# Kernel optimization log

Measured on AMD Instinct MI355X. Metric: run time of the kernel, lower is better.

## Reference

```python
import jax, jax.numpy as jnp
import numpy as np

V, E, H, DV = 32000, 512, 1024, 512
B, K = 64, 49


def setup_inputs():
    key = jax.random.key(0)
    ks = jax.random.split(key, 16)
    p = lambda i, shape: jax.random.normal(ks[i], shape, dtype=jnp.float32) * 0.02
    return {
        "thought": jax.random.normal(ks[0], (B, H), dtype=jnp.float32),
        "visual_features": jax.random.normal(ks[1], (B, K, DV), dtype=jnp.float32),
        "max_len": 64,
        "embedding": p(2, (V, E)),
        "Wih1": p(3, (4 * H, E)), "Whh1": p(4, (4 * H, H)),
        "bih1": jnp.zeros((4 * H,), jnp.float32), "bhh1": jnp.zeros((4 * H,), jnp.float32),
        "Wih2": p(5, (4 * H, H)), "Whh2": p(6, (4 * H, H)),
        "bih2": jnp.zeros((4 * H,), jnp.float32), "bhh2": jnp.zeros((4 * H,), jnp.float32),
        "Wg1": p(7, (H, H)), "bg1": jnp.zeros((H,), jnp.float32),
        "Wg2": p(8, (1, H)), "bg2": jnp.zeros((1,), jnp.float32),
        "Wo": p(9, (V, H)), "bo": jnp.zeros((V,), jnp.float32),
        "Wv": p(10, (H, DV)), "bv": jnp.zeros((H,), jnp.float32),
        "ln_g": jnp.ones((H,), jnp.float32), "ln_b": jnp.zeros((H,), jnp.float32),
    }


def _lstm_cell(x, h, c, Wih, Whh, bih, bhh):
    # PyTorch LSTM gate order: i, f, g, o
    z = x @ Wih.T + h @ Whh.T + bih + bhh
    i, f, g, o = jnp.split(z, 4, axis=-1)
    c_new = jax.nn.sigmoid(f) * c + jax.nn.sigmoid(i) * jnp.tanh(g)
    h_new = jax.nn.sigmoid(o) * jnp.tanh(c_new)
    return h_new, c_new


def reference(thought, visual_features, max_len, embedding, Wih1, Whh1, bih1, bhh1,
              Wih2, Whh2, bih2, bbh2=None, bih2_dummy=None, **_unused):
    raise RuntimeError('placeholder')


def reference(thought, visual_features, max_len, embedding, Wih1, Whh1, bih1, bhh1,
              Wih2, Whh2, bih2, bhh2, Wg1, bg1, Wg2, bg2, Wo, bo, Wv, bv, ln_g, ln_b):
    Bsz, Hd = thought.shape
    temperature = 0.4  # epoch = 0 -> 0.4 + 0.4*0
    top_p = 0.7        # epoch = 0 -> 0.7 + 0.2*0
    scale = 1.0 / jnp.sqrt(jnp.asarray(Hd, jnp.float32))
    # visual_proj: Linear + LayerNorm (Dropout is identity in eval mode)
    vp = visual_features @ Wv.T + bv
    mu = vp.mean(-1, keepdims=True)
    var = vp.var(-1, keepdims=True)
    vp = (vp - mu) / jnp.sqrt(var + 1e-5) * ln_g + ln_b  # [B,K,H]
    b_idx = jnp.arange(Bsz)
    # carry: (h1,c1,h2,c2, input token, last-3 token history, history validity)
    init = (thought, jnp.zeros_like(thought), thought, jnp.zeros_like(thought),
            jnp.full((Bsz,), 1, jnp.int32),
            jnp.zeros((Bsz, 3), jnp.int32), jnp.zeros((Bsz, 3), jnp.bool_))
    keys = jax.random.split(jax.random.key(42), max_len)

    def step(carry, key):
        h1, c1, h2, c2, inp, hist, histv = carry
        emb = embedding[inp]  # [B,E]
        h1, c1 = _lstm_cell(emb, h1, c1, Wih1, Whh1, bih1, bhh1)
        h2, c2 = _lstm_cell(h1, h2, c2, Wih2, Whh2, bih2, bhh2)
        gate = jax.nn.sigmoid(jnp.tanh(h2 @ Wg1.T + bg1) @ Wg2.T + bg2)  # [B,1]
        out = h2 * gate
        attn = jax.nn.softmax(jnp.einsum('bh,bkh->bk', out, vp) * scale, axis=-1)
        out = out + jnp.einsum('bk,bkh->bh', attn, vp)
        logits = out @ Wo.T + bo  # [B,V]
        # repetition penalty: -2.0 once per UNIQUE token in last-3 history (set semantics via .max)
        pen = jnp.zeros_like(logits).at[b_idx[:, None], hist].max(histv.astype(logits.dtype))
        logits = (logits - 2.0 * pen) / temperature
        # nucleus (top-p) filtering, matching top_k_top_p_filtering with top_k=0
        order = jnp.argsort(-logits, axis=-1)
        sl = jnp.take_along_axis(logits, order, axis=-1)
        cum = jnp.cumsum(jax.nn.softmax(sl, axis=-1), axis=-1)
        rem = cum > top_p
        rem = jnp.concatenate([jnp.zeros_like(rem[:, :1]), rem[:, :-1]], axis=-1)
        mask = jnp.zeros_like(rem).at[b_idx[:, None], order].set(rem)
        logits = jnp.where(mask, -jnp.inf, logits)
        nxt = jax.random.categorical(key, logits).astype(jnp.int32)  # multinomial sample
        hist = jnp.concatenate([hist[:, 1:], nxt[:, None]], axis=1)
        histv = jnp.concatenate([histv[:, 1:], jnp.ones((Bsz, 1), jnp.bool_)], axis=1)
        return (h1, c1, h2, c2, nxt, hist, histv), nxt

    _, toks = jax.lax.scan(step, init, keys)
    return toks.T  # [B, max_len]
```

## Files before the change

kernel.cpp:

```cpp
#include <hip/hip_runtime.h>
#include <hip/hip_bf16.h>
#include <stdint.h>


#define B_   64
#define H_   1024
#define E_   512
#define DV_  512
#define KV_  49
#define V_   32000
#define T_   64

__device__ __forceinline__ uint32_t rotl32(uint32_t x, int r) {
  return (x << r) | (x >> (32 - r));
}
__device__ __forceinline__ void tf2x32(uint32_t k0, uint32_t k1,
                                       uint32_t x0, uint32_t x1,
                                       uint32_t& o0, uint32_t& o1) {
  uint32_t ks0 = k0, ks1 = k1, ks2 = k0 ^ k1 ^ 0x1BD11BDAu;
  x0 += ks0; x1 += ks1;
#define RND_(r) { x0 += x1; x1 = rotl32(x1, r) ^ x0; }
  RND_(13) RND_(15) RND_(26) RND_(6)  x0 += ks1; x1 += ks2 + 1u;
  RND_(17) RND_(29) RND_(16) RND_(24) x0 += ks2; x1 += ks0 + 2u;
  RND_(13) RND_(15) RND_(26) RND_(6)  x0 += ks0; x1 += ks1 + 3u;
  RND_(17) RND_(29) RND_(16) RND_(24) x0 += ks1; x1 += ks2 + 4u;
  RND_(13) RND_(15) RND_(26) RND_(6)  x0 += ks2; x1 += ks0 + 5u;
#undef RND_
  o0 = x0; o1 = x1;
}

__device__ __forceinline__ unsigned key_of(float f) {
  unsigned u = __float_as_uint(f);
  return (u & 0x80000000u) ? ~u : (u | 0x80000000u);
}
__device__ __forceinline__ float sigf(float x) { return 1.0f / (1.0f + expf(-x)); }

template <int BN, int TM, int TN, int NTHR>
__global__ __launch_bounds__(NTHR)
void gemm_dq(const float* __restrict__ A0, int lda0, const float* __restrict__ W0,
             int ldw0, int K0, float* __restrict__ out0, int ldo0, int nt0,
             const float* __restrict__ A1, int lda1, const float* __restrict__ W1,
             int ldw1, int K1, float* __restrict__ out1, int ldo1) {
  constexpr int LD = 36;
  constexpr int ROWS = 64 + BN;
  constexpr int NF4 = ROWS * 8 / NTHR;
  constexpr int BUFST = ROWS * LD;
  constexpr int CG = BN / TN;
  static_assert(ROWS * 8 % NTHR == 0, "staging divisibility");
  static_assert((64 / TM) * CG == NTHR, "thread grid");
  static_assert(TN == 4, "float4 epilogue");
  __shared__ __align__(16) float S[2][ROWS][LD];

  const int tid = threadIdx.x;
  const int bx = blockIdx.x;
  const float* A; const float* W; float* out;
  int lda, ldw, K, ldo, n0;
  if (bx < nt0) { A = A0; W = W0; out = out0; lda = lda0; ldw = ldw0; K = K0; ldo = ldo0; n0 = bx * BN; }
  else          { A = A1; W = W1; out = out1; lda = lda1; ldw = ldw1; K = K1; ldo = ldo1; n0 = (bx - nt0) * BN; }
  const int m0 = blockIdx.y * 64;
  const int tc = tid % CG, tr = tid / CG;

  const float* gp[NF4];
  float* lp[NF4];
#pragma unroll
  for (int q = 0; q < NF4; ++q) {
    int l = tid + q * NTHR;
    int r = l >> 3, c4 = l & 7;
    gp[q] = (l < 512) ? (A + (m0 + r) * lda + c4 * 4)
                      : (W + (n0 + (r - 64)) * ldw + c4 * 4);
    lp[q] = &S[0][r][(c4 ^ ((r >> 2) & 7)) << 2];
  }

  float4 pre[NF4];
#pragma unroll
  for (int q = 0; q < NF4; ++q) pre[q] = *(const float4*)gp[q];
#pragma unroll
  for (int q = 0; q < NF4; ++q) *(float4*)lp[q] = pre[q];
  __syncthreads();

  float acc[TM][TN] = {};
  const int nch = K >> 5;
  for (int c = 0; c < nch; ++c) {
    const bool more = (c + 1 < nch);
    if (more) {
      const int kc = (c + 1) << 5;
#pragma unroll
      for (int q = 0; q < NF4; ++q) pre[q] = *(const float4*)(gp[q] + kc);
    }
    const float* Sb = &S[c & 1][0][0];
#pragma unroll
    for (int kk = 0; kk < 8; ++kk) {
      float4 a4[TM], w4[TN];
#pragma unroll
      for (int i = 0; i < TM; ++i) {
        int m = tr * TM + i;
        a4[i] = *(const float4*)(Sb + m * LD + ((kk ^ ((m >> 2) & 7)) << 2));
      }
#pragma unroll
      for (int j = 0; j < TN; ++j) {
        int rw = 64 + tc * TN + j;
        w4[j] = *(const float4*)(Sb + rw * LD + ((kk ^ ((rw >> 2) & 7)) << 2));
      }
#pragma unroll
      for (int i = 0; i < TM; ++i)
#pragma unroll
        for (int j = 0; j < TN; ++j) {
          acc[i][j] = fmaf(a4[i].x, w4[j].x, acc[i][j]);
          acc[i][j] = fmaf(a4[i].y, w4[j].y, acc[i][j]);
          acc[i][j] = fmaf(a4[i].z, w4[j].z, acc[i][j]);
          acc[i][j] = fmaf(a4[i].w, w4[j].w, acc[i][j]);
        }
    }
    if (more) {
      const int bo = ((c + 1) & 1) * BUFST;
#pragma unroll
      for (int q = 0; q < NF4; ++q) *(float4*)(lp[q] + bo) = pre[q];
    }
    __syncthreads();
  }

#pragma unroll
  for (int i = 0; i < TM; ++i) {
    float4 o;
    o.x = acc[i][0]; o.y = acc[i][1]; o.z = acc[i][2]; o.w = acc[i][3];
    *(float4*)&out[(m0 + tr * TM + i) * ldo + n0 + tc * TN] = o;
  }
}

__global__ __launch_bounds__(256)
void ln_vp(float* __restrict__ vp, const float* __restrict__ bv,
           const float* __restrict__ g, const float* __restrict__ bt) {
  int row = blockIdx.x, tid = threadIdx.x;
  __shared__ float buf[H_];
  __shared__ float red[256];
  float* p = vp + (long long)row * H_;
  for (int h = tid; h < H_; h += 256) buf[h] = __fadd_rn(p[h], bv[h]);
  __syncthreads();
  float s = 0;
  for (int h = tid; h < H_; h += 256) s += buf[h];
  red[tid] = s; __syncthreads();
  for (int off = 128; off > 0; off >>= 1) { if (tid < off) red[tid] += red[tid + off]; __syncthreads(); }
  float mu = red[0] / (float)H_;
  __syncthreads();
  float vs = 0;
  for (int h = tid; h < H_; h += 256) { float d = buf[h] - mu; vs += d * d; }
  red[tid] = vs; __syncthreads();
  for (int off = 128; off > 0; off >>= 1) { if (tid < off) red[tid] += red[tid + off]; __syncthreads(); }
  float var = red[0] / (float)H_;
  float sq = sqrtf(var + 1e-5f);
  for (int h = tid; h < H_; h += 256) {
    float nrm = __fdiv_rn(__fsub_rn(buf[h], mu), sq);
    p[h] = __fadd_rn(__fmul_rn(nrm, g[h]), bt[h]);
  }
}

__global__ __launch_bounds__(256)
void lstm_cell2(const float* __restrict__ dx, const float* __restrict__ dh,
                const float* __restrict__ bih, const float* __restrict__ bhh,
                float* __restrict__ c,
                float* __restrict__ hA, int ldA, float* __restrict__ hB, int ldB) {
  int idx = blockIdx.x * 256 + threadIdx.x;
  int b = idx >> 10, h = idx & 1023;
  float z[4];
#pragma unroll
  for (int g = 0; g < 4; g++) {
    int j = g * 1024 + h;
    float s = __fadd_rn(dx[b * 4096 + j], dh[b * 4096 + j]);
    s = __fadd_rn(s, bih[j]);
    s = __fadd_rn(s, bhh[j]);
    z[g] = s;
  }
  float fc = __fmul_rn(sigf(z[1]), c[idx]);
  float ig = __fmul_rn(sigf(z[0]), tanhf(z[2]));
  float cn = __fadd_rn(fc, ig);
  float hn = __fmul_rn(sigf(z[3]), tanhf(cn));
  c[idx] = cn;
  hA[(long long)b * ldA + h] = hn;
  hB[(long long)b * ldB + h] = hn;
}

__global__ __launch_bounds__(256)
void gate_attn(const float* __restrict__ dg, const float* __restrict__ bg1,
               const float* __restrict__ Wg2, const float* __restrict__ bg2,
               const float* __restrict__ h2buf, const float* __restrict__ vp,
               float* __restrict__ ctx) {
  int b = blockIdx.x, tid = threadIdx.x;
  __shared__ float t1[H_], outv[H_], attn[64];
  __shared__ float gate_s;
  for (int h = tid; h < H_; h += 256)
    t1[h] = tanhf(__fadd_rn(dg[b * H_ + h], bg1[h]));
  __syncthreads();
  if (tid == 0) {
    float s = 0;
    for (int h = 0; h < H_; h++) s = fmaf(t1[h], Wg2[h], s);
    gate_s = sigf(__fadd_rn(s, bg2[0]));
  }
  __syncthreads();
  float gate = gate_s;
  for (int h = tid; h < H_; h += 256) outv[h] = __fmul_rn(h2buf[b * H_ + h], gate);
  __syncthreads();
  if (tid < KV_) {
    const float* vrow = vp + ((long long)b * KV_ + tid) * H_;
    float a = 0;
    for (int h = 0; h < H_; h++) a = fmaf(outv[h], vrow[h], a);
    attn[tid] = __fmul_rn(a, 0.03125f);
  }
  __syncthreads();
  if (tid == 0) {
    float m = -INFINITY;
    for (int k = 0; k < KV_; k++) m = fmaxf(m, attn[k]);
    float ss = 0;
    for (int k = 0; k < KV_; k++) { attn[k] = expf(attn[k] - m); ss += attn[k]; }
    for (int k = 0; k < KV_; k++) attn[k] = __fdiv_rn(attn[k], ss);
  }
  __syncthreads();
  for (int h = tid; h < H_; h += 256) {
    float acc = 0;
    for (int k = 0; k < KV_; k++) acc = fmaf(attn[k], vp[((long long)b * KV_ + k) * H_ + h], acc);
    ctx[b * H_ + h] = __fadd_rn(outv[h], acc);
  }
}

__global__ __launch_bounds__(256)
void init_state(const float* __restrict__ thought, const float* __restrict__ embedding,
                float* c1, float* c2, float* xcat1, float* xcat2,
                int* hist, int* histv) {
  int i = blockIdx.x * 256 + threadIdx.x;
  if (i < B_ * H_) {
    int b = i >> 10, h = i & 1023;
    c1[i] = 0.f; c2[i] = 0.f;
    float th = thought[i];
    xcat1[b * (E_ + H_) + E_ + h] = th;
    xcat2[b * (2 * H_) + H_ + h] = th;
    if (h < E_) xcat1[b * (E_ + H_) + h] = embedding[E_ + h];
  }
  if (i < B_ * 3) { hist[i] = 0; histv[i] = 0; }
}

__global__ __launch_bounds__(1024)
void sample_kernel(const float* __restrict__ dlog, const float* __restrict__ bo,
                   float* __restrict__ Lbuf, float* __restrict__ Ebuf,
                   int* __restrict__ hist, int* __restrict__ histv,
                   const float* __restrict__ embedding, float* __restrict__ xcat1,
                   int* __restrict__ outTok, int t) {
  int b = blockIdx.x, tid = threadIdx.x;
  __shared__ float redf[1024];
  __shared__ int   redi[1024];
  __shared__ unsigned long long binS[256], suf[256];
  __shared__ unsigned binC[256];
  __shared__ int jstar_s;
  __shared__ unsigned long long carry_s;
  __shared__ unsigned prefix_s;

  int hh0 = hist[b * 3 + 0], hh1 = hist[b * 3 + 1], hh2 = hist[b * 3 + 2];
  int p0 = histv[b * 3 + 0] ? hh0 : -1;
  int p1 = histv[b * 3 + 1] ? hh1 : -1;
  int p2 = histv[b * 3 + 2] ? hh2 : -1;
  const float* pa = dlog + (long long)b * V_;
  float* L = Lbuf + (long long)b * V_;
  float* E = Ebuf + (long long)b * V_;

  float lm = -INFINITY;
  for (int v = tid; v < V_; v += 1024) {
    float raw = __fadd_rn(pa[v], bo[v]);
    if (v == p0 || v == p1 || v == p2) raw = __fsub_rn(raw, 2.0f);
    float l = __fdiv_rn(raw, 0.4f);
    L[v] = l;
    lm = fmaxf(lm, l);
  }
  redf[tid] = lm; __syncthreads();
  for (int off = 512; off > 0; off >>= 1) { if (tid < off) redf[tid] = fmaxf(redf[tid], redf[tid + off]); __syncthreads(); }
  float m = redf[0];
  __syncthreads();

  float ls = 0;
  for (int v = tid; v < V_; v += 1024) { float e = expf(L[v] - m); E[v] = e; ls += e; }
  redf[tid] = ls; __syncthreads();
  for (int off = 512; off > 0; off >>= 1) { if (tid < off) redf[tid] += redf[tid + off]; __syncthreads(); }
  float Z = redf[0];
  __syncthreads();

  const double SC = 17592186044416.0;
  const unsigned long long B0 =
      (unsigned long long)(0.699999988079071044921875 * 17592186044416.0);
  if (tid == 0) { carry_s = 0ull; prefix_s = 0u; }
  __syncthreads();
  for (int pass = 0; pass < 4; pass++) {
    int shift = 24 - 8 * pass;
    unsigned maskk = (pass == 0) ? 0u : (0xFFFFFFFFu << (shift + 8));
    if (tid < 256) { binS[tid] = 0ull; binC[tid] = 0u; }
    __syncthreads();
    unsigned pref = prefix_s;
    unsigned long long carry = carry_s;
    for (int v = tid; v < V_; v += 1024) {
      unsigned key = key_of(L[v]);
      if ((key & maskk) == pref) {
        unsigned bin = (key >> shift) & 255u;
        unsigned long long S = (unsigned long long)((double)(E[v] / Z) * SC);
        atomicAdd(&binS[bin], S);
        atomicAdd(&binC[bin], 1u);
      }
    }
    __syncthreads();
    if (tid < 256) suf[tid] = binS[tid];
    __syncthreads();
    for (int off = 1; off < 256; off <<= 1) {
      unsigned long long add = 0ull;
      if (tid < 256 && tid + off < 256) add = suf[tid + off];
      __syncthreads();
      if (tid < 256) suf[tid] += add;
      __syncthreads();
    }
    if (tid == 0) jstar_s = 256;
    __syncthreads();
    if (tid < 256 && binC[tid] > 0u) {
      unsigned long long A = carry + ((tid < 255) ? suf[tid + 1] : 0ull);
      if (A <= B0) atomicMin(&jstar_s, tid);
    }
    __syncthreads();
    if (tid == 0) {
      int j = jstar_s;
      carry_s = carry + ((j < 255) ? suf[j + 1] : 0ull);
      prefix_s = pref | (((unsigned)j) << shift);
    }
    __syncthreads();
  }
  unsigned Kstar = prefix_s;

  unsigned kt0, kt1;
  tf2x32(0u, 42u, 0u, (unsigned)t, kt0, kt1);

  float bestv = -INFINITY; int besti = 0x7fffffff;
  for (int v = tid; v < V_; v += 1024) {
    float l = L[v];
    if (key_of(l) >= Kstar) {
      unsigned r0, r1;
      tf2x32(kt0, kt1, 0u, (unsigned)(b * V_ + v), r0, r1);
      unsigned bits = r0 ^ r1;
      float u = __uint_as_float((bits >> 9) | 0x3f800000u) - 1.0f;
      u = fmaxf(u, 1.17549435e-38f);
      float gum = -logf(-logf(u));
      float val = __fadd_rn(l, gum);
      if (val > bestv) { bestv = val; besti = v; }
    }
  }
  redf[tid] = bestv; redi[tid] = besti; __syncthreads();
  for (int off = 512; off > 0; off >>= 1) {
    if (tid < off) {
      float ov = redf[tid + off]; int oi = redi[tid + off];
      if (ov > redf[tid] || (ov == redf[tid] && oi < redi[tid])) { redf[tid] = ov; redi[tid] = oi; }
    }
    __syncthreads();
  }
  int tok = redi[0];
  if (tid == 0) {
    outTok[b * T_ + t] = tok;
    hist[b * 3 + 0] = hh1; hist[b * 3 + 1] = hh2; hist[b * 3 + 2] = tok;
    int v1 = histv[b * 3 + 1], v2 = histv[b * 3 + 2];
    histv[b * 3 + 0] = v1; histv[b * 3 + 1] = v2; histv[b * 3 + 2] = 1;
  }
  for (int k = tid; k < E_; k += 1024)
    xcat1[b * (E_ + H_) + k] = embedding[(long long)tok * E_ + k];
}

extern "C" void kernel_launch(void* const* d_in, const int* in_sizes, int n_in,
                              void* d_out, int out_size, void* d_ws, size_t ws_size,
                              hipStream_t stream) {
  const float* thought   = (const float*)d_in[0];
  const float* visf      = (const float*)d_in[1];
  const float* embedding = (const float*)d_in[3];
  const float* Wih1 = (const float*)d_in[4];
  const float* Whh1 = (const float*)d_in[5];
  const float* bih1 = (const float*)d_in[6];
  const float* bhh1 = (const float*)d_in[7];
  const float* Wih2 = (const float*)d_in[8];
  const float* Whh2 = (const float*)d_in[9];
  const float* bih2 = (const float*)d_in[10];
  const float* bhh2 = (const float*)d_in[11];
  const float* Wg1  = (const float*)d_in[12];
  const float* bg1  = (const float*)d_in[13];
  const float* Wg2  = (const float*)d_in[14];
  const float* bg2  = (const float*)d_in[15];
  const float* Wo   = (const float*)d_in[16];
  const float* bo   = (const float*)d_in[17];
  const float* Wv   = (const float*)d_in[18];
  const float* bv   = (const float*)d_in[19];
  const float* ln_g = (const float*)d_in[20];
  const float* ln_b = (const float*)d_in[21];
  int* outTok = (int*)d_out;

  float* ws = (float*)d_ws;
  long long off = 0;
  float* vp    = ws + off; off += (long long)B_ * KV_ * H_;
  float* xcat1 = ws + off; off += B_ * (E_ + H_);
  float* xcat2 = ws + off; off += B_ * (2 * H_);
  float* c1    = ws + off; off += B_ * H_;
  float* c2    = ws + off; off += B_ * H_;
  float* h2buf = ws + off; off += B_ * H_;
  float* ctx   = ws + off; off += B_ * H_;
  float* dx    = ws + off; off += (long long)B_ * 4096;
  float* dh    = ws + off; off += (long long)B_ * 4096;
  float* dg    = ws + off; off += (long long)B_ * H_;
  float* dlog  = ws + off; off += (long long)B_ * V_;
  float* Lbuf  = ws + off; off += (long long)B_ * V_;
  float* Ebuf  = ws + off; off += (long long)B_ * V_;
  int* hist  = (int*)(ws + off); off += 256;
  int* histv = (int*)(ws + off); off += 256;

  init_state<<<256, 256, 0, stream>>>(thought, embedding, c1, c2, xcat1, xcat2, hist, histv);

  gemm_dq<128, 8, 4, 256><<<dim3(8, KV_), 256, 0, stream>>>(
      visf, DV_, Wv, DV_, DV_, vp, H_, 8,
      visf, DV_, Wv, DV_, DV_, vp, H_);
  ln_vp<<<B_ * KV_, 256, 0, stream>>>(vp, bv, ln_g, ln_b);

  for (int t = 0; t < T_; t++) {
    gemm_dq<32, 4, 4, 128><<<dim3(256, 1), 128, 0, stream>>>(
        xcat1, E_ + H_, Wih1, E_, E_, dx, 4096, 128,
        xcat1 + E_, E_ + H_, Whh1, H_, H_, dh, 4096);
    lstm_cell2<<<256, 256, 0, stream>>>(dx, dh, bih1, bhh1, c1,
                                        xcat1 + E_, E_ + H_, xcat2, 2 * H_);
    gemm_dq<32, 4, 4, 128><<<dim3(256, 1), 128, 0, stream>>>(
        xcat2, 2 * H_, Wih2, H_, H_, dx, 4096, 128,
        xcat2 + H_, 2 * H_, Whh2, H_, H_, dh, 4096);
    lstm_cell2<<<256, 256, 0, stream>>>(dx, dh, bih2, bhh2, c2,
                                        h2buf, H_, xcat2 + H_, 2 * H_);
    gemm_dq<32, 4, 4, 128><<<dim3(32, 1), 128, 0, stream>>>(
        h2buf, H_, Wg1, H_, H_, dg, H_, 32,
        h2buf, H_, Wg1, H_, H_, dg, H_);
    gate_attn<<<B_, 256, 0, stream>>>(dg, bg1, Wg2, bg2, h2buf, vp, ctx);
    gemm_dq<128, 8, 4, 256><<<dim3(250, 1), 256, 0, stream>>>(
        ctx, H_, Wo, H_, H_, dlog, V_, 250,
        ctx, H_, Wo, H_, H_, dlog, V_);
    sample_kernel<<<B_, 1024, 0, stream>>>(dlog, bo, Lbuf, Ebuf, hist, histv,
                                           embedding, xcat1, outTok, t);
  }
}
```

Measured before the change: 31.30 ms.

## Fuse all decode steps into one persistent megakernel with grid barriers

Replaces the per-timestep sequence of separate kernel launches (GEMMs, LSTM cells, gate/attention, sampling) with a single persistent kernel of 256 blocks that synchronises phases through a software global barrier. Sampling is split across four blocks per batch row, with partial histograms and argmax results exchanged through workspace buffers. The aim is to remove hundreds of launch overheads and tail gaps across the 64-step recurrence. In exchange, each block is limited to 256 threads and one block per CU, and the kernel depends on all 256 blocks being co-resident for the spin barrier to avoid deadlock.

```diff
diff --git a/kernel.cpp b/kernel.cpp
--- a/kernel.cpp
+++ b/kernel.cpp
@@ -1,5 +1,4 @@
 #include <hip/hip_runtime.h>
-#include <hip/hip_bf16.h>
 #include <stdint.h>
 
 
@@ -10,6 +9,7 @@
 #define KV_  49
 #define V_   32000
 #define T_   64
+#define NBLK 256
 
 __device__ __forceinline__ uint32_t rotl32(uint32_t x, int r) {
   return (x << r) | (x >> (32 - r));
@@ -35,12 +35,32 @@
 }
 __device__ __forceinline__ float sigf(float x) { return 1.0f / (1.0f + expf(-x)); }
 
+__device__ __forceinline__ void gsync(unsigned* bar) {
+  __syncthreads();
+  if (threadIdx.x == 0) {
+    __threadfence();
+    unsigned g = __hip_atomic_load(&bar[1], __ATOMIC_RELAXED, __HIP_MEMORY_SCOPE_AGENT);
+    unsigned a = __hip_atomic_fetch_add(&bar[0], 1u, __ATOMIC_ACQ_REL, __HIP_MEMORY_SCOPE_AGENT);
+    if (a + 1u == (unsigned)NBLK) {
+      __hip_atomic_store(&bar[0], 0u, __ATOMIC_RELAXED, __HIP_MEMORY_SCOPE_AGENT);
+      __hip_atomic_store(&bar[1], g + 1u, __ATOMIC_RELEASE, __HIP_MEMORY_SCOPE_AGENT);
+    } else {
+      while (__hip_atomic_load(&bar[1], __ATOMIC_ACQUIRE, __HIP_MEMORY_SCOPE_AGENT) == g)
+        __builtin_amdgcn_s_sleep(2);
+    }
+  }
+  __syncthreads();
+}
+
+__global__ void bar_init(unsigned* bar) {
+  if (threadIdx.x < 2) bar[threadIdx.x] = 0u;
+}
+
 template <int BN, int TM, int TN, int NTHR>
-__global__ __launch_bounds__(NTHR)
-void gemm_dq(const float* __restrict__ A0, int lda0, const float* __restrict__ W0,
-             int ldw0, int K0, float* __restrict__ out0, int ldo0, int nt0,
-             const float* __restrict__ A1, int lda1, const float* __restrict__ W1,
-             int ldw1, int K1, float* __restrict__ out1, int ldo1) {
+__device__ void gemm_tile(int tid, float* Sb0, int n0, int m0,
+                          const float* __restrict__ A, int lda,
+                          const float* __restrict__ W, int ldw, int K,
+                          float* __restrict__ out, int ldo) {
   constexpr int LD = 36;
   constexpr int ROWS = 64 + BN;
   constexpr int NF4 = ROWS * 8 / NTHR;
@@ -49,390 +69,480 @@
   static_assert(ROWS * 8 % NTHR == 0, "staging divisibility");
   static_assert((64 / TM) * CG == NTHR, "thread grid");
   static_assert(TN == 4, "float4 epilogue");
-  __shared__ __align__(16) float S[2][ROWS][LD];
-
-  const int tid = threadIdx.x;
-  const int bx = blockIdx.x;
-  const float* A; const float* W; float* out;
-  int lda, ldw, K, ldo, n0;
-  if (bx < nt0) { A = A0; W = W0; out = out0; lda = lda0; ldw = ldw0; K = K0; ldo = ldo0; n0 = bx * BN; }
-  else          { A = A1; W = W1; out = out1; lda = lda1; ldw = ldw1; K = K1; ldo = ldo1; n0 = (bx - nt0) * BN; }
-  const int m0 = blockIdx.y * 64;
+  const bool act = tid < NTHR;
   const int tc = tid % CG, tr = tid / CG;
-
   const float* gp[NF4];
   float* lp[NF4];
-#pragma unroll
-  for (int q = 0; q < NF4; ++q) {
-    int l = tid + q * NTHR;
-    int r = l >> 3, c4 = l & 7;
-    gp[q] = (l < 512) ? (A + (m0 + r) * lda + c4 * 4)
-                      : (W + (n0 + (r - 64)) * ldw + c4 * 4);
-    lp[q] = &S[0][r][(c4 ^ ((r >> 2) & 7)) << 2];
-  }
-
   float4 pre[NF4];
-#pragma unroll
-  for (int q = 0; q < NF4; ++q) pre[q] = *(const float4*)gp[q];
-#pragma unroll
-  for (int q = 0; q < NF4; ++q) *(float4*)lp[q] = pre[q];
+  if (act) {
+#pragma unroll
+    for (int q = 0; q < NF4; ++q) {
+      int l = tid + q * NTHR;
+      int r = l >> 3, c4 = l & 7;
+      gp[q] = (l < 512) ? (A + (m0 + r) * lda + c4 * 4)
+                        : (W + (n0 + (r - 64)) * ldw + c4 * 4);
+      lp[q] = Sb0 + r * LD + ((c4 ^ ((r >> 2) & 7)) << 2);
+    }
+#pragma unroll
+    for (int q = 0; q < NF4; ++q) pre[q] = *(const float4*)gp[q];
+#pragma unroll
+    for (int q = 0; q < NF4; ++q) *(float4*)lp[q] = pre[q];
+  }
   __syncthreads();
-
   float acc[TM][TN] = {};
   const int nch = K >> 5;
   for (int c = 0; c < nch; ++c) {
     const bool more = (c + 1 < nch);
-    if (more) {
+    if (act && more) {
       const int kc = (c + 1) << 5;
 #pragma unroll
       for (int q = 0; q < NF4; ++q) pre[q] = *(const float4*)(gp[q] + kc);
     }
-    const float* Sb = &S[c & 1][0][0];
-#pragma unroll
-    for (int kk = 0; kk < 8; ++kk) {
-      float4 a4[TM], w4[TN];
-#pragma unroll
-      for (int i = 0; i < TM; ++i) {
-        int m = tr * TM + i;
-        a4[i] = *(const float4*)(Sb + m * LD + ((kk ^ ((m >> 2) & 7)) << 2));
-      }
-#pragma unroll
-      for (int j = 0; j < TN; ++j) {
-        int rw = 64 + tc * TN + j;
-        w4[j] = *(const float4*)(Sb + rw * LD + ((kk ^ ((rw >> 2) & 7)) << 2));
-      }
-#pragma unroll
-      for (int i = 0; i < TM; ++i)
+    if (act) {
+      const float* Sb = Sb0 + (c & 1) * BUFST;
+#pragma unroll
+      for (int kk = 0; kk < 8; ++kk) {
+        float4 a4[TM], w4[TN];
+#pragma unroll
+        for (int i = 0; i < TM; ++i) {
+          int m = tr * TM + i;
+          a4[i] = *(const float4*)(Sb + m * LD + ((kk ^ ((m >> 2) & 7)) << 2));
+        }
 #pragma unroll
         for (int j = 0; j < TN; ++j) {
-          acc[i][j] = fmaf(a4[i].x, w4[j].x, acc[i][j]);
-          acc[i][j] = fmaf(a4[i].y, w4[j].y, acc[i][j]);
-          acc[i][j] = fmaf(a4[i].z, w4[j].z, acc[i][j]);
-          acc[i][j] = fmaf(a4[i].w, w4[j].w, acc[i][j]);
-        }
-    }
-    if (more) {
-      const int bo = ((c + 1) & 1) * BUFST;
-#pragma unroll
-      for (int q = 0; q < NF4; ++q) *(float4*)(lp[q] + bo) = pre[q];
+          int rw = 64 + tc * TN + j;
+          w4[j] = *(const float4*)(Sb + rw * LD + ((kk ^ ((rw >> 2) & 7)) << 2));
+        }
+#pragma unroll
+        for (int i = 0; i < TM; ++i)
+#pragma unroll
+          for (int j = 0; j < TN; ++j) {
+            acc[i][j] = fmaf(a4[i].x, w4[j].x, acc[i][j]);
+            acc[i][j] = fmaf(a4[i].y, w4[j].y, acc[i][j]);
+            acc[i][j] = fmaf(a4[i].z, w4[j].z, acc[i][j]);
+            acc[i][j] = fmaf(a4[i].w, w4[j].w, acc[i][j]);
+          }
+      }
+    }
+    if (act && more) {
+      const int bo2 = ((c + 1) & 1) * BUFST;
+#pragma unroll
+      for (int q = 0; q < NF4; ++q) *(float4*)(lp[q] + bo2) = pre[q];
     }
     __syncthreads();
   }
-
-#pragma unroll
-  for (int i = 0; i < TM; ++i) {
-    float4 o;
-    o.x = acc[i][0]; o.y = acc[i][1]; o.z = acc[i][2]; o.w = acc[i][3];
-    *(float4*)&out[(m0 + tr * TM + i) * ldo + n0 + tc * TN] = o;
-  }
-}
-
-__global__ __launch_bounds__(256)
-void ln_vp(float* __restrict__ vp, const float* __restrict__ bv,
-           const float* __restrict__ g, const float* __restrict__ bt) {
-  int row = blockIdx.x, tid = threadIdx.x;
-  __shared__ float buf[H_];
-  __shared__ float red[256];
-  float* p = vp + (long long)row * H_;
-  for (int h = tid; h < H_; h += 256) buf[h] = __fadd_rn(p[h], bv[h]);
-  __syncthreads();
-  float s = 0;
-  for (int h = tid; h < H_; h += 256) s += buf[h];
-  red[tid] = s; __syncthreads();
-  for (int off = 128; off > 0; off >>= 1) { if (tid < off) red[tid] += red[tid + off]; __syncthreads(); }
-  float mu = red[0] / (float)H_;
-  __syncthreads();
-  float vs = 0;
-  for (int h = tid; h < H_; h += 256) { float d = buf[h] - mu; vs += d * d; }
-  red[tid] = vs; __syncthreads();
-  for (int off = 128; off > 0; off >>= 1) { if (tid < off) red[tid] += red[tid + off]; __syncthreads(); }
-  float var = red[0] / (float)H_;
-  float sq = sqrtf(var + 1e-5f);
-  for (int h = tid; h < H_; h += 256) {
-    float nrm = __fdiv_rn(__fsub_rn(buf[h], mu), sq);
-    p[h] = __fadd_rn(__fmul_rn(nrm, g[h]), bt[h]);
-  }
-}
-
-__global__ __launch_bounds__(256)
-void lstm_cell2(const float* __restrict__ dx, const float* __restrict__ dh,
-                const float* __restrict__ bih, const float* __restrict__ bhh,
-                float* __restrict__ c,
-                float* __restrict__ hA, int ldA, float* __restrict__ hB, int ldB) {
-  int idx = blockIdx.x * 256 + threadIdx.x;
-  int b = idx >> 10, h = idx & 1023;
-  float z[4];
-#pragma unroll
-  for (int g = 0; g < 4; g++) {
-    int j = g * 1024 + h;
-    float s = __fadd_rn(dx[b * 4096 + j], dh[b * 4096 + j]);
-    s = __fadd_rn(s, bih[j]);
-    s = __fadd_rn(s, bhh[j]);
-    z[g] = s;
-  }
-  float fc = __fmul_rn(sigf(z[1]), c[idx]);
-  float ig = __fmul_rn(sigf(z[0]), tanhf(z[2]));
-  float cn = __fadd_rn(fc, ig);
-  float hn = __fmul_rn(sigf(z[3]), tanhf(cn));
-  c[idx] = cn;
-  hA[(long long)b * ldA + h] = hn;
-  hB[(long long)b * ldB + h] = hn;
-}
-
-__global__ __launch_bounds__(256)
-void gate_attn(const float* __restrict__ dg, const float* __restrict__ bg1,
-               const float* __restrict__ Wg2, const float* __restrict__ bg2,
-               const float* __restrict__ h2buf, const float* __restrict__ vp,
-               float* __restrict__ ctx) {
-  int b = blockIdx.x, tid = threadIdx.x;
-  __shared__ float t1[H_], outv[H_], attn[64];
-  __shared__ float gate_s;
-  for (int h = tid; h < H_; h += 256)
-    t1[h] = tanhf(__fadd_rn(dg[b * H_ + h], bg1[h]));
-  __syncthreads();
-  if (tid == 0) {
+  if (act) {
+#pragma unroll
+    for (int i = 0; i < TM; ++i) {
+      float4 o;
+      o.x = acc[i][0]; o.y = acc[i][1]; o.z = acc[i][2]; o.w = acc[i][3];
+      *(float4*)&out[(m0 + tr * TM + i) * ldo + n0 + tc * TN] = o;
+    }
+  }
+}
+
+struct LnLds   { float buf[H_]; float red[256]; };
+struct AttnLds { float t1[H_]; float outv[H_]; float attn[64]; float gate; };
+struct SamLds  {
+  float redf[256]; int redi[256];
+  unsigned long long whist[4][257];
+  unsigned long long suf[256];
+  unsigned long long wq[4];
+  unsigned long long carry;
+  unsigned prefix;
+  int jstar;
+};
+
+struct MegaP {
+  const float *thought, *visf, *embedding;
+  const float *Wih1, *Whh1, *bih1, *bhh1;
+  const float *Wih2, *Whh2, *bih2, *bhh2;
+  const float *Wg1, *bg1, *Wg2, *bg2;
+  const float *Wo, *bo, *Wv, *bv, *ln_g, *ln_b;
+  float *vp, *xcat1, *xcat2, *c1, *c2, *h2buf, *ctx, *dx, *dh, *dg, *dlog, *Lb, *Eb;
+  int *hist, *histv, *outTok;
+  float *pM, *pS, *pGv;
+  int *pGi;
+  unsigned long long *pH;
+  unsigned *bar;
+};
+
+__global__ __launch_bounds__(256, 1)
+void mega(MegaP p) {
+  __shared__ __align__(16) unsigned char LDSU_[55296];
+  float* GS = (float*)LDSU_;
+  const int bx = blockIdx.x;
+  const int tid = threadIdx.x;
+
+  {
+    int i = bx * 256 + tid;
+    if (i < B_ * H_) {
+      int b = i >> 10, h = i & 1023;
+      p.c1[i] = 0.f; p.c2[i] = 0.f;
+      float th = p.thought[i];
+      p.xcat1[b * (E_ + H_) + E_ + h] = th;
+      p.xcat2[b * (2 * H_) + H_ + h] = th;
+      if (h < E_) p.xcat1[b * (E_ + H_) + h] = p.embedding[E_ + h];
+    }
+    if (i < B_ * 3) { p.hist[i] = 0; p.histv[i] = 0; }
+  }
+  for (int s = bx; s < 8 * KV_; s += NBLK)
+    gemm_tile<128, 8, 4, 256>(tid, GS, (s & 7) * 128, (s >> 3) * 64,
+                              p.visf, DV_, p.Wv, DV_, DV_, p.vp, H_);
+  gsync(p.bar);
+
+  for (int row = bx; row < B_ * KV_; row += NBLK) {
+    LnLds& LL = *(LnLds*)LDSU_;
+    float* pp = p.vp + (long long)row * H_;
+    for (int h = tid; h < H_; h += 256) LL.buf[h] = __fadd_rn(pp[h], p.bv[h]);
+    __syncthreads();
     float s = 0;
-    for (int h = 0; h < H_; h++) s = fmaf(t1[h], Wg2[h], s);
-    gate_s = sigf(__fadd_rn(s, bg2[0]));
-  }
-  __syncthreads();
-  float gate = gate_s;
-  for (int h = tid; h < H_; h += 256) outv[h] = __fmul_rn(h2buf[b * H_ + h], gate);
-  __syncthreads();
-  if (tid < KV_) {
-    const float* vrow = vp + ((long long)b * KV_ + tid) * H_;
-    float a = 0;
-    for (int h = 0; h < H_; h++) a = fmaf(outv[h], vrow[h], a);
-    attn[tid] = __fmul_rn(a, 0.03125f);
-  }
-  __syncthreads();
-  if (tid == 0) {
-    float m = -INFINITY;
-    for (int k = 0; k < KV_; k++) m = fmaxf(m, attn[k]);
-    float ss = 0;
-    for (int k = 0; k < KV_; k++) { attn[k] = expf(attn[k] - m); ss += attn[k]; }
-    for (int k = 0; k < KV_; k++) attn[k] = __fdiv_rn(attn[k], ss);
-  }
-  __syncthreads();
-  for (int h = tid; h < H_; h += 256) {
-    float acc = 0;
-    for (int k = 0; k < KV_; k++) acc = fmaf(attn[k], vp[((long long)b * KV_ + k) * H_ + h], acc);
-    ctx[b * H_ + h] = __fadd_rn(outv[h], acc);
-  }
-}
-
-__global__ __launch_bounds__(256)
-void init_state(const float* __restrict__ thought, const float* __restrict__ embedding,
-                float* c1, float* c2, float* xcat1, float* xcat2,
-                int* hist, int* histv) {
-  int i = blockIdx.x * 256 + threadIdx.x;
-  if (i < B_ * H_) {
-    int b = i >> 10, h = i & 1023;
-    c1[i] = 0.f; c2[i] = 0.f;
-    float th = thought[i];
-    xcat1[b * (E_ + H_) + E_ + h] = th;
-    xcat2[b * (2 * H_) + H_ + h] = th;
-    if (h < E_) xcat1[b * (E_ + H_) + h] = embedding[E_ + h];
-  }
-  if (i < B_ * 3) { hist[i] = 0; histv[i] = 0; }
-}
-
-__global__ __launch_bounds__(1024)
-void sample_kernel(const float* __restrict__ dlog, const float* __restrict__ bo,
-                   float* __restrict__ Lbuf, float* __restrict__ Ebuf,
-                   int* __restrict__ hist, int* __restrict__ histv,
-                   const float* __restrict__ embedding, float* __restrict__ xcat1,
-                   int* __restrict__ outTok, int t) {
-  int b = blockIdx.x, tid = threadIdx.x;
-  __shared__ float redf[1024];
-  __shared__ int   redi[1024];
-  __shared__ unsigned long long binS[256], suf[256];
-  __shared__ unsigned binC[256];
-  __shared__ int jstar_s;
-  __shared__ unsigned long long carry_s;
-  __shared__ unsigned prefix_s;
-
-  int hh0 = hist[b * 3 + 0], hh1 = hist[b * 3 + 1], hh2 = hist[b * 3 + 2];
-  int p0 = histv[b * 3 + 0] ? hh0 : -1;
-  int p1 = histv[b * 3 + 1] ? hh1 : -1;
-  int p2 = histv[b * 3 + 2] ? hh2 : -1;
-  const float* pa = dlog + (long long)b * V_;
-  float* L = Lbuf + (long long)b * V_;
-  float* E = Ebuf + (long long)b * V_;
-
-  float lm = -INFINITY;
-  for (int v = tid; v < V_; v += 1024) {
-    float raw = __fadd_rn(pa[v], bo[v]);
-    if (v == p0 || v == p1 || v == p2) raw = __fsub_rn(raw, 2.0f);
-    float l = __fdiv_rn(raw, 0.4f);
-    L[v] = l;
-    lm = fmaxf(lm, l);
-  }
-  redf[tid] = lm; __syncthreads();
-  for (int off = 512; off > 0; off >>= 1) { if (tid < off) redf[tid] = fmaxf(redf[tid], redf[tid + off]); __syncthreads(); }
-  float m = redf[0];
-  __syncthreads();
-
-  float ls = 0;
-  for (int v = tid; v < V_; v += 1024) { float e = expf(L[v] - m); E[v] = e; ls += e; }
-  redf[tid] = ls; __syncthreads();
-  for (int off = 512; off > 0; off >>= 1) { if (tid < off) redf[tid] += redf[tid + off]; __syncthreads(); }
-  float Z = redf[0];
-  __syncthreads();
-
-  const double SC = 17592186044416.0;
-  const unsigned long long B0 =
-      (unsigned long long)(0.699999988079071044921875 * 17592186044416.0);
-  if (tid == 0) { carry_s = 0ull; prefix_s = 0u; }
-  __syncthreads();
-  for (int pass = 0; pass < 4; pass++) {
-    int shift = 24 - 8 * pass;
-    unsigned maskk = (pass == 0) ? 0u : (0xFFFFFFFFu << (shift + 8));
-    if (tid < 256) { binS[tid] = 0ull; binC[tid] = 0u; }
+    for (int h = tid; h < H_; h += 256) s += LL.buf[h];
+    LL.red[tid] = s; __syncthreads();
+    for (int off = 128; off > 0; off >>= 1) { if (tid < off) LL.red[tid] += LL.red[tid + off]; __syncthreads(); }
+    float mu = LL.red[0] / (float)H_;
     __syncthreads();
-    unsigned pref = prefix_s;
-    unsigned long long carry = carry_s;
-    for (int v = tid; v < V_; v += 1024) {
-      unsigned key = key_of(L[v]);
-      if ((key & maskk) == pref) {
-        unsigned bin = (key >> shift) & 255u;
-        unsigned long long S = (unsigned long long)((double)(E[v] / Z) * SC);
-        atomicAdd(&binS[bin], S);
-        atomicAdd(&binC[bin], 1u);
-      }
+    float vs = 0;
+    for (int h = tid; h < H_; h += 256) { float d = LL.buf[h] - mu; vs += d * d; }
+    LL.red[tid] = vs; __syncthreads();
+    for (int off = 128; off > 0; off >>= 1) { if (tid < off) LL.red[tid] += LL.red[tid + off]; __syncthreads(); }
+    float var = LL.red[0] / (float)H_;
+    float sq = sqrtf(var + 1e-5f);
+    for (int h = tid; h < H_; h += 256) {
+      float nrm = __fdiv_rn(__fsub_rn(LL.buf[h], mu), sq);
+      pp[h] = __fadd_rn(__fmul_rn(nrm, p.ln_g[h]), p.ln_b[h]);
     }
     __syncthreads();
-    if (tid < 256) suf[tid] = binS[tid];
-    __syncthreads();
-    for (int off = 1; off < 256; off <<= 1) {
-      unsigned long long add = 0ull;
-      if (tid < 256 && tid + off < 256) add = suf[tid + off];
-      __syncthreads();
-      if (tid < 256) suf[tid] += add;
-      __syncthreads();
-    }
-    if (tid == 0) jstar_s = 256;
-    __syncthreads();
-    if (tid < 256 && binC[tid] > 0u) {
-      unsigned long long A = carry + ((tid < 255) ? suf[tid + 1] : 0ull);
-      if (A <= B0) atomicMin(&jstar_s, tid);
-    }
-    __syncthreads();
-    if (tid == 0) {
-      int j = jstar_s;
-      carry_s = carry + ((j < 255) ? suf[j + 1] : 0ull);
-      prefix_s = pref | (((unsigned)j) << shift);
-    }
-    __syncthreads();
-  }
-  unsigned Kstar = prefix_s;
-
-  unsigned kt0, kt1;
-  tf2x32(0u, 42u, 0u, (unsigned)t, kt0, kt1);
-
-  float bestv = -INFINITY; int besti = 0x7fffffff;
-  for (int v = tid; v < V_; v += 1024) {
-    float l = L[v];
-    if (key_of(l) >= Kstar) {
-      unsigned r0, r1;
-      tf2x32(kt0, kt1, 0u, (unsigned)(b * V_ + v), r0, r1);
-      unsigned bits = r0 ^ r1;
-      float u = __uint_as_float((bits >> 9) | 0x3f800000u) - 1.0f;
-      u = fmaxf(u, 1.17549435e-38f);
-      float gum = -logf(-logf(u));
-      float val = __fadd_rn(l, gum);
-      if (val > bestv) { bestv = val; besti = v; }
-    }
-  }
-  redf[tid] = bestv; redi[tid] = besti; __syncthreads();
-  for (int off = 512; off > 0; off >>= 1) {
-    if (tid < off) {
-      float ov = redf[tid + off]; int oi = redi[tid + off];
-      if (ov > redf[tid] || (ov == redf[tid] && oi < redi[tid])) { redf[tid] = ov; redi[tid] = oi; }
-    }
-    __syncthreads();
-  }
-  int tok = redi[0];
-  if (tid == 0) {
-    outTok[b * T_ + t] = tok;
-    hist[b * 3 + 0] = hh1; hist[b * 3 + 1] = hh2; hist[b * 3 + 2] = tok;
-    int v1 = histv[b * 3 + 1], v2 = histv[b * 3 + 2];
-    histv[b * 3 + 0] = v1; histv[b * 3 + 1] = v2; histv[b * 3 + 2] = 1;
-  }
-  for (int k = tid; k < E_; k += 1024)
-    xcat1[b * (E_ + H_) + k] = embedding[(long long)tok * E_ + k];
+  }
+  gsync(p.bar);
+
+  for (int t = 0; t < T_; ++t) {
+    if (bx < 128)
+      gemm_tile<32, 4, 4, 128>(tid, GS, bx * 32, 0,
+                               p.xcat1, E_ + H_, p.Wih1, E_, E_, p.dx, 4096);
+    else
+      gemm_tile<32, 4, 4, 128>(tid, GS, (bx - 128) * 32, 0,
+                               p.xcat1 + E_, E_ + H_, p.Whh1, H_, H_, p.dh, 4096);
+    gsync(p.bar);
+    {
+      int idx = bx * 256 + tid;
+      int b = idx >> 10, h = idx & 1023;
+      float z[4];
+#pragma unroll
+      for (int g = 0; g < 4; g++) {
+        int j = g * 1024 + h;
+        float s = __fadd_rn(p.dx[b * 4096 + j], p.dh[b * 4096 + j]);
+        s = __fadd_rn(s, p.bih1[j]);
+        s = __fadd_rn(s, p.bhh1[j]);
+        z[g] = s;
+      }
+      float fc = __fmul_rn(sigf(z[1]), p.c1[idx]);
+      float ig = __fmul_rn(sigf(z[0]), tanhf(z[2]));
+      float cn = __fadd_rn(fc, ig);
+      float hn = __fmul_rn(sigf(z[3]), tanhf(cn));
+      p.c1[idx] = cn;
+      p.xcat1[(long long)b * (E_ + H_) + E_ + h] = hn;
+      p.xcat2[(long long)b * (2 * H_) + h] = hn;
+    }
+    gsync(p.bar);
+    if (bx < 128)
+      gemm_tile<32, 4, 4, 128>(tid, GS, bx * 32, 0,
+                               p.xcat2, 2 * H_, p.Wih2, H_, H_, p.dx, 4096);
+    else
+      gemm_tile<32, 4, 4, 128>(tid, GS, (bx - 128) * 32, 0,
+                               p.xcat2 + H_, 2 * H_, p.Whh2, H_, H_, p.dh, 4096);
+    gsync(p.bar);
+    {
+      int idx = bx * 256 + tid;
+      int b = idx >> 10, h = idx & 1023;
+      float z[4];
+#pragma unroll
+      for (int g = 0; g < 4; g++) {
+        int j = g * 1024 + h;
+        float s = __fadd_rn(p.dx[b * 4096 + j], p.dh[b * 4096 + j]);
+        s = __fadd_rn(s, p.bih2[j]);
+        s = __fadd_rn(s, p.bhh2[j]);
+        z[g] = s;
+      }
+      float fc = __fmul_rn(sigf(z[1]), p.c2[idx]);
+      float ig = __fmul_rn(sigf(z[0]), tanhf(z[2]));
+      float cn = __fadd_rn(fc, ig);
+      float hn = __fmul_rn(sigf(z[3]), tanhf(cn));
+      p.c2[idx] = cn;
+      p.h2buf[(long long)b * H_ + h] = hn;
+      p.xcat2[(long long)b * (2 * H_) + H_ + h] = hn;
+    }
+    gsync(p.bar);
+    if (bx < 32)
+      gemm_tile<32, 4, 4, 128>(tid, GS, bx * 32, 0,
+                               p.h2buf, H_, p.Wg1, H_, H_, p.dg, H_);
+    gsync(p.bar);
+    if (bx < B_) {
+      AttnLds& AL = *(AttnLds*)LDSU_;
+      int b = bx;
+      for (int h = tid; h < H_; h += 256)
+        AL.t1[h] = tanhf(__fadd_rn(p.dg[b * H_ + h], p.bg1[h]));
+      __syncthreads();
+      if (tid == 0) {
+        float s = 0;
+        for (int h = 0; h < H_; h++) s = fmaf(AL.t1[h], p.Wg2[h], s);
+        AL.gate = sigf(__fadd_rn(s, p.bg2[0]));
+      }
+      __syncthreads();
+      float gate = AL.gate;
+      for (int h = tid; h < H_; h += 256) AL.outv[h] = __fmul_rn(p.h2buf[b * H_ + h], gate);
+      __syncthreads();
+      if (tid < KV_) {
+        const float* vrow = p.vp + ((long long)b * KV_ + tid) * H_;
+        float a = 0;
+        for (int h = 0; h < H_; h++) a = fmaf(AL.outv[h], vrow[h], a);
+        AL.attn[tid] = __fmul_rn(a, 0.03125f);
+      }
+      __syncthreads();
+      if (tid == 0) {
+        float m = -INFINITY;
+        for (int k = 0; k < KV_; k++) m = fmaxf(m, AL.attn[k]);
+        float ss = 0;
+        for (int k = 0; k < KV_; k++) { AL.attn[k] = expf(AL.attn[k] - m); ss += AL.attn[k]; }
+        for (int k = 0; k < KV_; k++) AL.attn[k] = __fdiv_rn(AL.attn[k], ss);
+      }
+      __syncthreads();
+      for (int h = tid; h < H_; h += 256) {
+        float acc = 0;
+        for (int k = 0; k < KV_; k++) acc = fmaf(AL.attn[k], p.vp[((long long)b * KV_ + k) * H_ + h], acc);
+        p.ctx[b * H_ + h] = __fadd_rn(AL.outv[h], acc);
+      }
+    }
+    gsync(p.bar);
+    if (bx < 250)
+      gemm_tile<128, 8, 4, 256>(tid, GS, bx * 128, 0,
+                                p.ctx, H_, p.Wo, H_, H_, p.dlog, V_);
+    gsync(p.bar);
+
+    {
+      const int b = bx >> 2, role = bx & 3;
+      const int gtid = (role << 8) | tid;
+      SamLds& SL = *(SamLds*)LDSU_;
+      int hh0 = p.hist[b * 3 + 0], hh1 = p.hist[b * 3 + 1], hh2 = p.hist[b * 3 + 2];
+      int q0 = p.histv[b * 3 + 0] ? hh0 : -1;
+      int q1 = p.histv[b * 3 + 1] ? hh1 : -1;
+      int q2 = p.histv[b * 3 + 2] ? hh2 : -1;
+      const float* pa = p.dlog + (long long)b * V_;
+      float* L = p.Lb + (long long)b * V_;
+      float* E = p.Eb + (long long)b * V_;
+
+      float lm = -INFINITY;
+      for (int v = gtid; v < V_; v += 1024) {
+        float raw = __fadd_rn(pa[v], p.bo[v]);
+        if (v == q0 || v == q1 || v == q2) raw = __fsub_rn(raw, 2.0f);
+        float l = __fdiv_rn(raw, 0.4f);
+        L[v] = l;
+        lm = fmaxf(lm, l);
+      }
+      p.pM[(b * 4 + role) * 256 + tid] = lm;
+      gsync(p.bar);
+      {
+        const float* s0 = p.pM + (b * 4 + 0) * 256;
+        const float* s1 = p.pM + (b * 4 + 1) * 256;
+        const float* s2 = p.pM + (b * 4 + 2) * 256;
+        const float* s3 = p.pM + (b * 4 + 3) * 256;
+        SL.redf[tid] = fmaxf(fmaxf(s0[tid], s2[tid]), fmaxf(s1[tid], s3[tid]));
+      }
+      __syncthreads();
+      for (int off = 128; off > 0; off >>= 1) { if (tid < off) SL.redf[tid] = fmaxf(SL.redf[tid], SL.redf[tid + off]); __syncthreads(); }
+      float m = SL.redf[0];
+      __syncthreads();
+
+      float ls = 0;
+      for (int v = gtid; v < V_; v += 1024) { float e = expf(L[v] - m); E[v] = e; ls += e; }
+      p.pS[(b * 4 + role) * 256 + tid] = ls;
+      gsync(p.bar);
+      {
+        const float* s0 = p.pS + (b * 4 + 0) * 256;
+        const float* s1 = p.pS + (b * 4 + 1) * 256;
+        const float* s2 = p.pS + (b * 4 + 2) * 256;
+        const float* s3 = p.pS + (b * 4 + 3) * 256;
+        SL.redf[tid] = (s0[tid] + s2[tid]) + (s1[tid] + s3[tid]);
+      }
+      __syncthreads();
+      for (int off = 128; off > 0; off >>= 1) { if (tid < off) SL.redf[tid] += SL.redf[tid + off]; __syncthreads(); }
+      float Z = SL.redf[0];
+      __syncthreads();
+
+      const double SC = 17592186044416.0;
+      const unsigned long long B0 =
+          (unsigned long long)(0.699999988079071044921875 * 17592186044416.0);
+      if (tid == 0) { SL.carry = 0ull; SL.prefix = 0u; }
+      __syncthreads();
+      for (int pass = 0; pass < 4; pass++) {
+        int shift = 24 - 8 * pass;
+        unsigned maskk = (pass == 0) ? 0u : (0xFFFFFFFFu << (shift + 8));
+        for (int i = tid; i < 4 * 257; i += 256) ((unsigned long long*)SL.whist)[i] = 0ull;
+        __syncthreads();
+        unsigned pref = SL.prefix;
+        unsigned long long carry = SL.carry;
+        for (int v = gtid; v < V_; v += 1024) {
+          unsigned key = key_of(L[v]);
+          if ((key & maskk) == pref) {
+            unsigned bin = (key >> shift) & 255u;
+            unsigned long long S = (unsigned long long)((double)(E[v] / Z) * SC);
+            atomicAdd(&SL.whist[tid >> 6][bin], (S << 16) | 1ull);
+          }
+        }
+        __syncthreads();
+        {
+          unsigned long long part =
+              ((SL.whist[0][tid] + SL.whist[1][tid]) + SL.whist[2][tid]) + SL.whist[3][tid];
+          p.pH[((pass * B_ + b) * 4 + role) * 256 + tid] = part;
+        }
+        gsync(p.bar);
+        unsigned long long bs =
+            ((p.pH[((pass * B_ + b) * 4 + 0) * 256 + tid] +
+              p.pH[((pass * B_ + b) * 4 + 1) * 256 + tid]) +
+             p.pH[((pass * B_ + b) * 4 + 2) * 256 + tid]) +
+            p.pH[((pass * B_ + b) * 4 + 3) * 256 + tid];
+        if (tid == 0) SL.jstar = 256;
+        __syncthreads();
+        unsigned long long sown = bs >> 16;
+        unsigned long long sincl = sown;
+#pragma unroll
+        for (int off = 1; off < 64; off <<= 1) {
+          unsigned long long o = __shfl_down(sincl, off);
+          if ((tid & 63) + off < 64) sincl += o;
+        }
+        if ((tid & 63) == 0) SL.wq[tid >> 6] = sincl;
+        __syncthreads();
+        {
+          unsigned long long add = 0ull;
+          for (int w2 = (tid >> 6) + 1; w2 < 4; ++w2) add += SL.wq[w2];
+          SL.suf[tid] = sincl + add - sown;
+        }
+        __syncthreads();
+        if ((unsigned)(bs & 0xFFFFull) > 0u) {
+          unsigned long long A = carry + SL.suf[tid];
+          if (A <= B0) atomicMin(&SL.jstar, tid);
+        }
+        __syncthreads();
+        if (tid == 0) {
+          int j = SL.jstar;
+          SL.carry = carry + SL.suf[j];
+          SL.prefix = pref | (((unsigned)j) << shift);
+        }
+        __syncthreads();
+      }
+      unsigned Kstar = SL.prefix;
+
+      unsigned kt0, kt1;
+      tf2x32(0u, 42u, 0u, (unsigned)t, kt0, kt1);
+
+      float bestv = -INFINITY; int besti = 0x7fffffff;
+      for (int v = gtid; v < V_; v += 1024) {
+        float l = L[v];
+        if (key_of(l) >= Kstar) {
+          unsigned r0, r1;
+          tf2x32(kt0, kt1, 0u, (unsigned)(b * V_ + v), r0, r1);
+          unsigned bits = r0 ^ r1;
+          float u = __uint_as_float((bits >> 9) | 0x3f800000u) - 1.0f;
+          u = fmaxf(u, 1.17549435e-38f);
+          float gum = -logf(-logf(u));
+          float val = __fadd_rn(l, gum);
+          if (val > bestv) { bestv = val; besti = v; }
+        }
+      }
+      p.pGv[(b * 4 + role) * 256 + tid] = bestv;
+      p.pGi[(b * 4 + role) * 256 + tid] = besti;
+      gsync(p.bar);
+      {
+        const float* v0 = p.pGv + (b * 4 + 0) * 256;
+        const float* v1 = p.pGv + (b * 4 + 1) * 256;
+        const float* v2 = p.pGv + (b * 4 + 2) * 256;
+        const float* v3 = p.pGv + (b * 4 + 3) * 256;
+        const int* i0 = p.pGi + (b * 4 + 0) * 256;
+        const int* i1 = p.pGi + (b * 4 + 1) * 256;
+        const int* i2 = p.pGi + (b * 4 + 2) * 256;
+        const int* i3 = p.pGi + (b * 4 + 3) * 256;
+        float av = v0[tid]; int ai = i0[tid];
+        float ov = v2[tid]; int oi = i2[tid];
+        if (ov > av || (ov == av && oi < ai)) { av = ov; ai = oi; }
+        float bv = v1[tid]; int bi = i1[tid];
+        ov = v3[tid]; oi = i3[tid];
+        if (ov > bv || (ov == bv && oi < bi)) { bv = ov; bi = oi; }
+        if (bv > av || (bv == av && bi < ai)) { av = bv; ai = bi; }
+        SL.redf[tid] = av; SL.redi[tid] = ai;
+      }
+      __syncthreads();
+      for (int off = 128; off > 0; off >>= 1) {
+        if (tid < off) {
+          float ov = SL.redf[tid + off]; int oi = SL.redi[tid + off];
+          if (ov > SL.redf[tid] || (ov == SL.redf[tid] && oi < SL.redi[tid])) { SL.redf[tid] = ov; SL.redi[tid] = oi; }
+        }
+        __syncthreads();
+      }
+      int tok = SL.redi[0];
+      if (role == 0 && tid == 0) {
+        p.outTok[b * T_ + t] = tok;
+        p.hist[b * 3 + 0] = hh1; p.hist[b * 3 + 1] = hh2; p.hist[b * 3 + 2] = tok;
+        int v1h = p.histv[b * 3 + 1], v2h = p.histv[b * 3 + 2];
+        p.histv[b * 3 + 0] = v1h; p.histv[b * 3 + 1] = v2h; p.histv[b * 3 + 2] = 1;
+      }
+      if (gtid < E_)
+        p.xcat1[b * (E_ + H_) + gtid] = p.embedding[(long long)tok * E_ + gtid];
+    }
+    gsync(p.bar);
+  }
 }
 
 extern "C" void kernel_launch(void* const* d_in, const int* in_sizes, int n_in,
                               void* d_out, int out_size, void* d_ws, size_t ws_size,
                               hipStream_t stream) {
-  const float* thought   = (const float*)d_in[0];
-  const float* visf      = (const float*)d_in[1];
-  const float* embedding = (const float*)d_in[3];
-  const float* Wih1 = (const float*)d_in[4];
-  const float* Whh1 = (const float*)d_in[5];
-  const float* bih1 = (const float*)d_in[6];
-  const float* bhh1 = (const float*)d_in[7];
-  const float* Wih2 = (const float*)d_in[8];
-  const float* Whh2 = (const float*)d_in[9];
-  const float* bih2 = (const float*)d_in[10];
-  const float* bhh2 = (const float*)d_in[11];
-  const float* Wg1  = (const float*)d_in[12];
-  const float* bg1  = (const float*)d_in[13];
-  const float* Wg2  = (const float*)d_in[14];
-  const float* bg2  = (const float*)d_in[15];
-  const float* Wo   = (const float*)d_in[16];
-  const float* bo   = (const float*)d_in[17];
-  const float* Wv   = (const float*)d_in[18];
-  const float* bv   = (const float*)d_in[19];
-  const float* ln_g = (const float*)d_in[20];
-  const float* ln_b = (const float*)d_in[21];
-  int* outTok = (int*)d_out;
+  MegaP p;
+  p.thought   = (const float*)d_in[0];
+  p.visf      = (const float*)d_in[1];
+  p.embedding = (const float*)d_in[3];
+  p.Wih1 = (const float*)d_in[4];
+  p.Whh1 = (const float*)d_in[5];
+  p.bih1 = (const float*)d_in[6];
+  p.bhh1 = (const float*)d_in[7];
+  p.Wih2 = (const float*)d_in[8];
+  p.Whh2 = (const float*)d_in[9];
+  p.bih2 = (const float*)d_in[10];
+  p.bhh2 = (const float*)d_in[11];
+  p.Wg1  = (const float*)d_in[12];
+  p.bg1  = (const float*)d_in[13];
+  p.Wg2  = (const float*)d_in[14];
+  p.bg2  = (const float*)d_in[15];
+  p.Wo   = (const float*)d_in[16];
+  p.bo   = (const float*)d_in[17];
+  p.Wv   = (const float*)d_in[18];
+  p.bv   = (const float*)d_in[19];
+  p.ln_g = (const float*)d_in[20];
+  p.ln_b = (const float*)d_in[21];
+  p.outTok = (int*)d_out;
 
   float* ws = (float*)d_ws;
   long long off = 0;
-  float* vp    = ws + off; off += (long long)B_ * KV_ * H_;
-  float* xcat1 = ws + off; off += B_ * (E_ + H_);
-  float* xcat2 = ws + off; off += B_ * (2 * H_);
-  float* c1    = ws + off; off += B_ * H_;
-  float* c2    = ws + off; off += B_ * H_;
-  float* h2buf = ws + off; off += B_ * H_;
-  float* ctx   = ws + off; off += B_ * H_;
-  float* dx    = ws + off; off += (long long)B_ * 4096;
-  float* dh    = ws + off; off += (long long)B_ * 4096;
-  float* dg    = ws + off; off += (long long)B_ * H_;
-  float* dlog  = ws + off; off += (long long)B_ * V_;
-  float* Lbuf  = ws + off; off += (long long)B_ * V_;
-  float* Ebuf  = ws + off; off += (long long)B_ * V_;
-  int* hist  = (int*)(ws + off); off += 256;
-  int* histv = (int*)(ws + off); off += 256;
-
-  init_state<<<256, 256, 0, stream>>>(thought, embedding, c1, c2, xcat1, xcat2, hist, histv);
-
-  gemm_dq<128, 8, 4, 256><<<dim3(8, KV_), 256, 0, stream>>>(
-      visf, DV_, Wv, DV_, DV_, vp, H_, 8,
-      visf, DV_, Wv, DV_, DV_, vp, H_);
-  ln_vp<<<B_ * KV_, 256, 0, stream>>>(vp, bv, ln_g, ln_b);
-
-  for (int t = 0; t < T_; t++) {
-    gemm_dq<32, 4, 4, 128><<<dim3(256, 1), 128, 0, stream>>>(
-        xcat1, E_ + H_, Wih1, E_, E_, dx, 4096, 128,
-        xcat1 + E_, E_ + H_, Whh1, H_, H_, dh, 4096);
-    lstm_cell2<<<256, 256, 0, stream>>>(dx, dh, bih1, bhh1, c1,
-                                        xcat1 + E_, E_ + H_, xcat2, 2 * H_);
-    gemm_dq<32, 4, 4, 128><<<dim3(256, 1), 128, 0, stream>>>(
-        xcat2, 2 * H_, Wih2, H_, H_, dx, 4096, 128,
-        xcat2 + H_, 2 * H_, Whh2, H_, H_, dh, 4096);
-    lstm_cell2<<<256, 256, 0, stream>>>(dx, dh, bih2, bhh2, c2,
-                                        h2buf, H_, xcat2 + H_, 2 * H_);
-    gemm_dq<32, 4, 4, 128><<<dim3(32, 1), 128, 0, stream>>>(
-        h2buf, H_, Wg1, H_, H_, dg, H_, 32,
-        h2buf, H_, Wg1, H_, H_, dg, H_);
-    gate_attn<<<B_, 256, 0, stream>>>(dg, bg1, Wg2, bg2, h2buf, vp, ctx);
-    gemm_dq<128, 8, 4, 256><<<dim3(250, 1), 256, 0, stream>>>(
-        ctx, H_, Wo, H_, H_, dlog, V_, 250,
-        ctx, H_, Wo, H_, H_, dlog, V_);
-    sample_kernel<<<B_, 1024, 0, stream>>>(dlog, bo, Lbuf, Ebuf, hist, histv,
-                                           embedding, xcat1, outTok, t);
-  }
-}
+  p.vp    = ws + off; off += (long long)B_ * KV_ * H_;
+  p.xcat1 = ws + off; off += B_ * (E_ + H_);
+  p.xcat2 = ws + off; off += B_ * (2 * H_);
+  p.c1    = ws + off; off += B_ * H_;
+  p.c2    = ws + off; off += B_ * H_;
+  p.h2buf = ws + off; off += B_ * H_;
+  p.ctx   = ws + off; off += B_ * H_;
+  p.dx    = ws + off; off += (long long)B_ * 4096;
+  p.dh    = ws + off; off += (long long)B_ * 4096;
+  p.dg    = ws + off; off += (long long)B_ * H_;
+  p.dlog  = ws + off; off += (long long)B_ * V_;
+  p.Lb    = ws + off; off += (long long)B_ * V_;
+  p.Eb    = ws + off; off += (long long)B_ * V_;
+  p.hist  = (int*)(ws + off); off += 256;
+  p.histv = (int*)(ws + off); off += 256;
+  p.pM    = ws + off; off += B_ * 4 * 256;
+  p.pS    = ws + off; off += B_ * 4 * 256;
+  p.pGv   = ws + off; off += B_ * 4 * 256;
+  p.pGi   = (int*)(ws + off); off += B_ * 4 * 256;
+  p.pH    = (unsigned long long*)(ws + off); off += (long long)4 * B_ * 4 * 256 * 2;
+  p.bar   = (unsigned*)(ws + off); off += 64;
+
+  bar_init<<<1, 64, 0, stream>>>(p.bar);
+  mega<<<NBLK, 256, 0, stream>>>(p);
+}
```

After: 78.87 ms. 152% more time.
